# Performance work log

Hardware: AMD Instinct MI355X
Metric: run time of the kernel (lower is better)

Reference implementation:

```python
import jax, jax.numpy as jnp
import numpy as np


def _head_configs(n_heads, patch_num):
    candidates = set()
    for d in range(1, patch_num + 1):
        for K in (3, 5, 7):
            eff = (K - 1) * d + 1
            if eff <= patch_num and K <= patch_num and (K % 2 == 1):
                candidates.add((K, d, eff))
    gk = patch_num if patch_num % 2 == 1 else patch_num - 1
    gk = max(1, gk)
    candidates.add((gk, 1, gk))
    cand = sorted(candidates, key=lambda x: (x[2], -x[0], x[1]))
    if not cand:
        return [(1, 1)] * n_heads
    configs = []
    for h in range(n_heads):
        idx = round(h * (len(cand) - 1) / max(1, n_heads - 1))
        idx = min(idx, len(cand) - 1)
        configs.append((cand[idx][0], cand[idx][1]))
    return configs


def _build_na_mask(n_heads, patch_num):
    # [H, N, N] bool: True where key position is a (dilated) neighbor of query
    mask = np.zeros((n_heads, patch_num, patch_num), dtype=bool)
    pos = np.arange(patch_num)
    for h, (K, d) in enumerate(_head_configs(n_heads, patch_num)):
        off = (np.arange(K) - K // 2) * d
        ideal = pos[:, None] + off[None, :]          # [N, K]
        nb = np.clip(ideal, 0, patch_num - 1)
        valid = (ideal >= 0) & (ideal < patch_num)
        rows = np.repeat(pos, K)
        mask[h, rows[valid.ravel()], nb.ravel()[valid.ravel()]] = True
    return mask


N_HEADS = 16
PATCH_NUM = 1024
HEAD_DIM = 64
BATCH = 8


def setup_inputs() -> dict:
    key = jax.random.key(0)
    kq, kk, kv = jax.random.split(key, 3)
    shape = (BATCH, PATCH_NUM, N_HEADS, HEAD_DIM)  # [B, L, H, E]
    queries = jax.random.normal(kq, shape, dtype=jnp.float32)
    keys = jax.random.normal(kk, shape, dtype=jnp.float32)
    values = jax.random.normal(kv, shape, dtype=jnp.float32)
    na_mask = jnp.asarray(_build_na_mask(N_HEADS, PATCH_NUM))  # [H, N, N] bool
    return {"queries": queries, "keys": keys, "values": values, "na_mask": na_mask}


def reference(queries, keys, values, na_mask):
    B, L, H, E = queries.shape
    scale = E ** (-0.5)
    q = jnp.transpose(queries, (0, 2, 1, 3))  # [B, H, N, E]
    k = jnp.transpose(keys, (0, 2, 1, 3))
    v = jnp.transpose(values, (0, 2, 1, 3))
    attn = jnp.einsum('bhne,bhme->bhnm', q, k) * scale  # [B, H, N, N]
    attn = jnp.where(na_mask[None], attn, -jnp.inf)
    attn = jax.nn.softmax(attn, axis=-1)
    out = jnp.einsum('bhnm,bhme->bhne', attn, v)
    return jnp.transpose(out, (0, 2, 1, 3))  # [B, L, H, E]
```

## Files before the change

### kernel.cpp

```cpp
#include <hip/hip_runtime.h>

#define B_ 8
#define L_ 1024
#define H_ 16
#define E_ 64
#define HE_ (H_ * E_)

__constant__ int HHALF[16] = {1, 1, 1, 1, 3, 1, 1, 3, 1, 2, 3, 1, 2, 3, 2, 1};
__constant__ int HD[16]    = {1, 35, 69, 103, 46, 171, 205, 80, 273, 154, 114, 375, 205, 148, 239, 511};

template <int CTRL>
__device__ __forceinline__ float dpp_add(float x) {
    int moved = __builtin_amdgcn_update_dpp(0, __float_as_int(x), CTRL, 0xf, 0xf, false);
    return x + __int_as_float(moved);
}
__device__ __forceinline__ float row16_sum(float x) {
    x = dpp_add<0x121>(x);
    x = dpp_add<0x122>(x);
    x = dpp_add<0x124>(x);
    x = dpp_add<0x128>(x);
    return x;
}

__device__ __forceinline__ void gl4(float4& dst, const float* p) {
    asm volatile("global_load_dwordx4 %0, %1, off" : "=v"(dst) : "v"(p));
}

template <int HALF>
__device__ __forceinline__ void run_head(const float* __restrict__ Q,
                                         const float* __restrict__ Kp,
                                         const float* __restrict__ Vp,
                                         float* __restrict__ O,
                                         int rowbase, int q, int Dh)
{
    constexpr int NS = 2 * HALF + 1;
    const int qoff = rowbase + q * HE_;

    int  moff[NS];
    bool val[NS];
#pragma unroll
    for (int jj = 0; jj < NS; ++jj) {
        const int j = jj - HALF;
        const int m = q + j * Dh;
        val[jj] = (m >= 0) && (m < L_);
        const int mc = m < 0 ? 0 : (m >= L_ ? L_ - 1 : m);
        moff[jj] = rowbase + mc * HE_;
    }

    float4 qv, kv[NS], vv[NS];
    gl4(qv, Q + qoff);
#pragma unroll
    for (int jj = 0; jj < NS; ++jj) gl4(kv[jj], Kp + moff[jj]);
#pragma unroll
    for (int jj = 0; jj < NS; ++jj) gl4(vv[jj], Vp + moff[jj]);

    asm volatile("s_waitcnt vmcnt(%0)" :: "n"(NS) : "memory");
    __builtin_amdgcn_sched_barrier(0);

    float sc[NS];
#pragma unroll
    for (int jj = 0; jj < NS; ++jj) {
        float d = qv.x * kv[jj].x + qv.y * kv[jj].y + qv.z * kv[jj].z + qv.w * kv[jj].w;
        d = row16_sum(d);
        sc[jj] = val[jj] ? d * 0.125f : -1e30f;
    }

    float mx = sc[0];
#pragma unroll
    for (int jj = 1; jj < NS; ++jj) mx = fmaxf(mx, sc[jj]);
    float e[NS];
    float sum = 0.f;
#pragma unroll
    for (int jj = 0; jj < NS; ++jj) {
        e[jj] = __expf(sc[jj] - mx);
        sum += e[jj];
    }
    const float inv = 1.f / sum;

    asm volatile("s_waitcnt vmcnt(0)" ::: "memory");
    __builtin_amdgcn_sched_barrier(0);

    float4 acc = make_float4(0.f, 0.f, 0.f, 0.f);
#pragma unroll
    for (int jj = 0; jj < NS; ++jj) {
        const float w = e[jj] * inv;
        acc.x += w * vv[jj].x;
        acc.y += w * vv[jj].y;
        acc.z += w * vv[jj].z;
        acc.w += w * vv[jj].w;
    }

    *reinterpret_cast<float4*>(O + qoff) = acc;
}

__global__ __launch_bounds__(256, 4)
void msna_fwd(const float* __restrict__ Q, const float* __restrict__ Kp,
              const float* __restrict__ Vp, float* __restrict__ O)
{
    const int nwg = B_ * H_ * (L_ / 16);
    const int cpx = nwg >> 3;
    int blk = blockIdx.x;
    blk = (blk & 7) * cpx + (blk >> 3);

    const int tid  = threadIdx.x;
    const int lane = tid & 15;
    const int qi   = tid >> 4;
    const int qt   = blk & 63;
    const int h    = (blk >> 6) & 15;
    const int b    = blk >> 10;
    const int q    = qt * 16 + qi;

    const int Dh = HD[h];
    const int hf = HHALF[h];
    const int rowbase = b * (L_ * HE_) + h * E_ + 4 * lane;

    if (hf == 1)      run_head<1>(Q, Kp, Vp, O, rowbase, q, Dh);
    else if (hf == 2) run_head<2>(Q, Kp, Vp, O, rowbase, q, Dh);
    else              run_head<3>(Q, Kp, Vp, O, rowbase, q, Dh);
}

extern "C" void kernel_launch(void* const* d_in, const int* in_sizes, int n_in,
                              void* d_out, int out_size, void* d_ws, size_t ws_size,
                              hipStream_t stream)
{
    const float* Q = (const float*)d_in[0];
    const float* K = (const float*)d_in[1];
    const float* V = (const float*)d_in[2];
    float* O = (float*)d_out;

    const int blocks = B_ * H_ * (L_ / 16);
    msna_fwd<<<blocks, 256, 0, stream>>>(Q, K, V, O);
}
```

Measured before the change: 25.21 us.

## Group queries by dilation residue so workgroups share neighbor K/V rows

Workgroup-to-query mapping changes from contiguous query tiles to per-head groups where the 16 queries in a block are strided by the head's dilation (q = r + t*Dh). Queries in a block therefore share many of the same dilated key/value rows, which is meant to improve cache reuse for heads with large dilation. The grid is padded per head (1096 groups per batch), so some lanes do redundant clamped work with their stores masked off. Batch is now the low bits of the block index.

```diff
diff --git a/kernel.cpp b/kernel.cpp
--- a/kernel.cpp
+++ b/kernel.cpp
@@ -5,9 +5,12 @@
 #define H_ 16
 #define E_ 64
 #define HE_ (H_ * E_)
+#define NGRP_ 1096
 
 __constant__ int HHALF[16] = {1, 1, 1, 1, 3, 1, 1, 3, 1, 2, 3, 1, 2, 3, 2, 1};
 __constant__ int HD[16]    = {1, 35, 69, 103, 46, 171, 205, 80, 273, 154, 114, 375, 205, 148, 239, 511};
+__constant__ int HC[16]    = {1024, 30, 15, 10, 23, 6, 5, 13, 4, 7, 9, 3, 5, 7, 5, 3};
+__constant__ int HBASE[16] = {0, 64, 130, 195, 260, 327, 392, 457, 522, 591, 659, 724, 795, 860, 925, 1000};
 
 template <int CTRL>
 __device__ __forceinline__ float dpp_add(float x) {
@@ -31,7 +34,7 @@
                                          const float* __restrict__ Kp,
                                          const float* __restrict__ Vp,
                                          float* __restrict__ O,
-                                         int rowbase, int q, int Dh)
+                                         int rowbase, int q, int Dh, bool active)
 {
     constexpr int NS = 2 * HALF + 1;
     const int qoff = rowbase + q * HE_;
@@ -90,33 +93,46 @@
         acc.w += w * vv[jj].w;
     }
 
-    *reinterpret_cast<float4*>(O + qoff) = acc;
+    if (active)
+        *reinterpret_cast<float4*>(O + qoff) = acc;
 }
 
 __global__ __launch_bounds__(256, 4)
 void msna_fwd(const float* __restrict__ Q, const float* __restrict__ Kp,
               const float* __restrict__ Vp, float* __restrict__ O)
 {
-    const int nwg = B_ * H_ * (L_ / 16);
-    const int cpx = nwg >> 3;
-    int blk = blockIdx.x;
-    blk = (blk & 7) * cpx + (blk >> 3);
+    const int x   = blockIdx.x;
+    const int b   = x & 7;
+    const int rem = x >> 3;
+
+    constexpr int kCum[16] = {0, 64, 130, 195, 260, 327, 392, 457, 522, 591,
+                              659, 724, 795, 860, 925, 1000};
+    int h = 0;
+#pragma unroll
+    for (int i = 1; i < 16; ++i) h += (rem >= kCum[i]) ? 1 : 0;
+
+    const int g = rem - HBASE[h];
 
     const int tid  = threadIdx.x;
     const int lane = tid & 15;
-    const int qi   = tid >> 4;
-    const int qt   = blk & 63;
-    const int h    = (blk >> 6) & 15;
-    const int b    = blk >> 10;
-    const int q    = qt * 16 + qi;
+    const int slot = tid >> 4;
 
+    const unsigned vi = (unsigned)(g * 16 + slot);
+    const unsigned C  = (unsigned)HC[h];
+    const unsigned r  = vi / C;
+    const unsigned t  = vi - r * C;
     const int Dh = HD[h];
+
+    int q = (int)r + (int)t * Dh;
+    const bool active = (q < L_);
+    q = active ? q : (L_ - 1);
+
+    const int rowbase = b * (L_ * HE_) + h * E_ + 4 * lane;
     const int hf = HHALF[h];
-    const int rowbase = b * (L_ * HE_) + h * E_ + 4 * lane;
 
-    if (hf == 1)      run_head<1>(Q, Kp, Vp, O, rowbase, q, Dh);
-    else if (hf == 2) run_head<2>(Q, Kp, Vp, O, rowbase, q, Dh);
-    else              run_head<3>(Q, Kp, Vp, O, rowbase, q, Dh);
+    if (hf == 1)      run_head<1>(Q, Kp, Vp, O, rowbase, q, Dh, active);
+    else if (hf == 2) run_head<2>(Q, Kp, Vp, O, rowbase, q, Dh, active);
+    else              run_head<3>(Q, Kp, Vp, O, rowbase, q, Dh, active);
 }
 
 extern "C" void kernel_launch(void* const* d_in, const int* in_sizes, int n_in,
@@ -128,6 +144,6 @@
     const float* V = (const float*)d_in[2];
     float* O = (float*)d_out;
 
-    const int blocks = B_ * H_ * (L_ / 16);
+    const int blocks = B_ * NGRP_;
     msna_fwd<<<blocks, 256, 0, stream>>>(Q, K, V, O);
 }
```

Measured after the change: 25.41 us. About the same (+0.8%).
